# Optimization experiments

Measured on AMD Instinct MI355X. Metric: run time of the kernel, lower is better.

Reference implementation:

```python
import jax, jax.numpy as jnp
import numpy as np
from jax import lax

T, B, D_IN, H = 512, 128, 512, 512


def setup_inputs() -> dict:
    key = jax.random.key(0)
    k1, k2, k3, k4 = jax.random.split(key, 4)
    ins = jax.random.normal(k1, (T, B, D_IN), dtype=jnp.float32)
    resets = jax.random.bernoulli(k2, 0.05, (T, B))  # episode-boundary reset mask
    carry = jnp.zeros((B, H), dtype=jnp.float32)
    # fused GRU weights: gate order (r, z, n); input denses have no bias in flax GRUCell
    Wi = jax.random.normal(k3, (D_IN, 3 * H), dtype=jnp.float32) * (1.0 / np.sqrt(D_IN))
    Wh = jax.random.normal(k4, (H, 3 * H), dtype=jnp.float32) * (1.0 / np.sqrt(H))
    bh = jnp.zeros((3 * H,), dtype=jnp.float32)
    return {"carry": carry, "ins": ins, "resets": resets, "Wi": Wi, "Wh": Wh, "bh": bh}


def reference(carry, ins, resets, Wi, Wh, bh):
    """ScannedRNN forward: scan a flax GRUCell over time with per-step reset masking.

    Returns (final_carry [B,H], ys [T,B,H]).
    """

    def step(h, xr):
        x, r_mask = xr                       # x: [B,D_in], r_mask: [B]
        h = jnp.where(r_mask[:, None], jnp.zeros_like(h), h)
        gi = x @ Wi                          # [B,3H]  (no input bias in flax GRUCell)
        gh = h @ Wh + bh                     # [B,3H]
        ir, iz, inn = jnp.split(gi, 3, axis=-1)
        hr, hz, hn = jnp.split(gh, 3, axis=-1)
        r = jax.nn.sigmoid(ir + hr)
        z = jax.nn.sigmoid(iz + hz)
        n = jnp.tanh(inn + r * hn)
        new_h = (1.0 - z) * n + z * h
        return new_h, new_h                  # GRUCell returns (new_carry, new_carry)

    final_carry, ys = lax.scan(step, carry, (ins, resets))
    return final_carry, ys
```

## Files before the change

### kernel.cpp

```cpp
#include <hip/hip_runtime.h>

#define T_STEPS 512
#define BATCH   128
#define DIN     512
#define HDIM    512
#define THREEH  1536
#define THREADS 256
#define LDK     520
#define LDG     49
#define NGROUP  4
#define NSLICE  32
#define BC      32
#define HC      16
#define NC      48
#define CNT_STRIDE 16
#define FLAG_STRIDE 4
#define SPIN_MAX (1 << 22)
#define EX_DWORDS (NSLICE * BATCH * HC / 2)
#define DEC_OFF    2048
#define EX_OFF     4096
#define GI_OFF     (1u<<20)
#define GI_BYTES   201326592ULL

typedef _Float16 half8 __attribute__((ext_vector_type(8)));
typedef _Float16 half4v __attribute__((ext_vector_type(4)));
typedef float    f32x4 __attribute__((ext_vector_type(4)));
typedef unsigned int uint4v __attribute__((ext_vector_type(4)));

__global__ void sniff_kernel(const unsigned int* __restrict__ w,
                             unsigned int* __restrict__ dec) {
  unsigned int local = 0;
  for (int i = threadIdx.x; i < (T_STEPS * BATCH) / 4; i += THREADS) {
    if (w[i] > 1u) local = 1u;
  }
  if (local) atomicOr(dec, 1u);
}

__device__ __forceinline__ void run_gemm(const _Float16* __restrict__ sAa,
                                         const _Float16* __restrict__ sW,
                                         float* __restrict__ sAcc,
                                         int wid, int lane) {
  const int fr = lane & 15;
  const int kb = (lane >> 4) * 8;
  for (int tile = wid; tile < 6; tile += 4) {
    int mi = tile / 3, ni = tile - mi * 3;
    const _Float16* ap = sAa + (mi * 16 + fr) * LDK + kb;
    const _Float16* bp = sW  + (ni * 16 + fr) * LDK + kb;
    f32x4 acc = {0.f, 0.f, 0.f, 0.f};
#pragma unroll
    for (int kk = 0; kk < DIN / 32; ++kk)
      acc = __builtin_amdgcn_mfma_f32_16x16x32_f16(
          *(const half8*)(ap + kk * 32),
          *(const half8*)(bp + kk * 32), acc, 0, 0, 0);
    int crow = mi * 16 + (lane >> 4) * 4;
    int ccol = ni * 16 + fr;
#pragma unroll
    for (int j = 0; j < 4; ++j) sAcc[(crow + j) * LDG + ccol] = acc[j];
  }
}

__global__ __launch_bounds__(THREADS, 1)
void gru_kernel_v1(const float* __restrict__ carry,
                   const float* __restrict__ ins,
                   const void*  __restrict__ resets_raw,
                   const float* __restrict__ Wi,
                   const float* __restrict__ Wh,
                   const float* __restrict__ bh,
                   float* __restrict__ out,
                   unsigned int* __restrict__ cnt,
                   unsigned int* __restrict__ ex0,
                   unsigned int* __restrict__ ex1,
                   const unsigned int* __restrict__ dec)
{
  __shared__ alignas(16) _Float16 sWi[NC * LDK];
  __shared__ alignas(16) _Float16 sWh[NC * LDK];
  __shared__ alignas(16) _Float16 sA [BC * LDK];
  __shared__ float sGi[BC * LDG];
  __shared__ float sGh[BC * LDG];
  __shared__ float sBh[NC];
  __shared__ int   sRst[BC];

  const int tid  = threadIdx.x;
  const int bid  = blockIdx.x;
  const int g    = bid & (NGROUP - 1);
  const int p    = bid >> 2;
  const int row0 = g * BC;
  const int col0 = p * HC;

  float* carryOut = out;
  float* ys = out + BATCH * HDIM;

  const unsigned int isBool = *dec;
  const unsigned char* r8  = (const unsigned char*)resets_raw;
  const int*           r32 = (const int*)resets_raw;

  unsigned int* ex[2] = { ex0, ex1 };
  unsigned int* myCnt = cnt + g * CNT_STRIDE;

  for (int idx = tid; idx < DIN * NC; idx += THREADS) {
    int k  = idx / NC;
    int ci = idx - k * NC;
    int gcol = (ci >> 4) * HDIM + col0 + (ci & 15);
    sWi[ci * LDK + k] = (_Float16)Wi[k * THREEH + gcol];
    sWh[ci * LDK + k] = (_Float16)Wh[k * THREEH + gcol];
  }
  if (tid < NC) {
    int gcol = (tid >> 4) * HDIM + col0 + (tid & 15);
    sBh[tid] = bh[gcol];
  }

  float hreg[2];
  {
    int idx = tid * 2;
    int b0 = idx >> 4, c0 = idx & 15;
    hreg[0] = carry[(size_t)(row0 + b0) * HDIM + col0 + c0];
    hreg[1] = carry[(size_t)(row0 + b0) * HDIM + col0 + c0 + 1];
  }

  const int wid  = tid >> 6;
  const int lane = tid & 63;

  auto stageRst = [&](int t) {
    if (tid < BC) {
      int off = t * BATCH + row0 + tid;
      sRst[tid] = isBool ? (int)r8[off] : r32[off];
    }
  };
  auto stageX = [&](int t) {
    const float4* src = (const float4*)(ins + (size_t)(t * BATCH + row0) * DIN);
    for (int i = tid; i < BC * (DIN / 4); i += THREADS) {
      int r = i >> 7, c4 = i & 127;
      float4 v = src[(size_t)r * 128 + c4];
      half4v hv = {(_Float16)v.x, (_Float16)v.y, (_Float16)v.z, (_Float16)v.w};
      *(half4v*)&sA[r * LDK + c4 * 4] = hv;
    }
  };

  stageRst(0);
  stageX(0);
  __syncthreads();
  run_gemm(sA, sWi, sGi, wid, lane);
  __syncthreads();
  {
    const float4* src = (const float4*)(carry + (size_t)row0 * HDIM);
    for (int i = tid; i < BC * (HDIM / 4); i += THREADS) {
      int r = i >> 7, c4 = i & 127;
      float4 v = src[(size_t)r * 128 + c4];
      float m = sRst[r] ? 0.f : 1.f;
      half4v hv = {(_Float16)(v.x*m), (_Float16)(v.y*m),
                   (_Float16)(v.z*m), (_Float16)(v.w*m)};
      *(half4v*)&sA[r * LDK + c4 * 4] = hv;
    }
  }
  __syncthreads();

  for (int t = 0; t < T_STEPS; ++t) {
    if (t > 0) {
      {
        const unsigned int target = 32u * (unsigned)t;
        unsigned int fv;
        for (int it = 0; it < SPIN_MAX; ++it) {
          asm volatile("global_load_dword %0, %1, off sc0 sc1\n\t"
                       "s_waitcnt vmcnt(0)"
                       : "=v"(fv) : "v"(myCnt) : "memory");
          if (fv >= target) break;
          __builtin_amdgcn_s_sleep(1);
        }
      }
      {
        const unsigned int* exsrc = ex[(t - 1) & 1];
        uint4v vv[8];
#pragma unroll
        for (int j = 0; j < 8; ++j) {
          int i = tid + THREADS * j;
          int p_ = i >> 6, b_ = (i >> 1) & 31, hw = (i & 1) << 2;
          const unsigned int* sp = exsrc + p_ * 1024 + (row0 + b_) * 8 + hw;
          asm volatile("global_load_dwordx4 %0, %1, off sc0 sc1"
                       : "=&v"(vv[j]) : "v"(sp) : "memory");
        }
        asm volatile("s_waitcnt vmcnt(0)" ::: "memory");
        __builtin_amdgcn_sched_barrier(0);
#pragma unroll
        for (int j = 0; j < 8; ++j) {
          int i = tid + THREADS * j;
          int p_ = i >> 6, b_ = (i >> 1) & 31, hw = (i & 1) << 3;
          half8 hv = *reinterpret_cast<half8*>(&vv[j]);
          half8 z = {(_Float16)0, (_Float16)0, (_Float16)0, (_Float16)0,
                     (_Float16)0, (_Float16)0, (_Float16)0, (_Float16)0};
          hv = sRst[b_] ? z : hv;
          *(half8*)&sA[b_ * LDK + p_ * 16 + hw] = hv;
        }
      }
      __syncthreads();
    }

    run_gemm(sA, sWh, sGh, wid, lane);
    __syncthreads();

    {
#pragma unroll
      for (int e = 0; e < 2; ++e) {
        int idx = tid * 2 + e;
        int b = idx >> 4, cj = idx & 15;
        float gir = sGi[b * LDG + cj];
        float giz = sGi[b * LDG + 16 + cj];
        float gin = sGi[b * LDG + 32 + cj];
        float ghr = sGh[b * LDG + cj]      + sBh[cj];
        float ghz = sGh[b * LDG + 16 + cj] + sBh[16 + cj];
        float ghn = sGh[b * LDG + 32 + cj] + sBh[32 + cj];
        float r = 1.f / (1.f + __expf(-(gir + ghr)));
        float z = 1.f / (1.f + __expf(-(giz + ghz)));
        float n = tanhf(gin + r * ghn);
        float hp = sRst[b] ? 0.f : hreg[e];
        hreg[e] = (1.f - z) * n + z * hp;
      }
      union { _Float16 h[2]; unsigned int u; } pk;
      pk.h[0] = (_Float16)hreg[0];
      pk.h[1] = (_Float16)hreg[1];
      unsigned int* dst = ex[t & 1] + p * 1024 + (row0 + (tid >> 3)) * 8 + (tid & 7);
      asm volatile("global_store_dword %0, %1, off sc0 sc1"
                   :: "v"(dst), "v"(pk.u) : "memory");
      int b0 = (tid * 2) >> 4, c0 = (tid * 2) & 15;
      float2 yv = make_float2(hreg[0], hreg[1]);
      *(float2*)&ys[((size_t)t * BATCH + row0 + b0) * HDIM + col0 + c0] = yv;
      if (t == T_STEPS - 1)
        *(float2*)&carryOut[(size_t)(row0 + b0) * HDIM + col0 + c0] = yv;
    }
    asm volatile("s_waitcnt vmcnt(0)" ::: "memory");
    __syncthreads();
    if (tid == 0) atomicAdd(myCnt, 1u);

    if (t < T_STEPS - 1) {
      stageRst(t + 1);
      stageX(t + 1);
      __syncthreads();
      run_gemm(sA, sWi, sGi, wid, lane);
      __syncthreads();
    }
  }
}

__global__ __launch_bounds__(256, 1)
void gi_prepass2(const float* __restrict__ ins,
                 const float* __restrict__ Wi,
                 _Float16* __restrict__ gis)
{
  __shared__ alignas(16) _Float16 sWiT[48 * LDK];
  __shared__ alignas(16) _Float16 sX[32 * LDK];

  const int tid = threadIdx.x;
  const int bid = blockIdx.x;
  const int n   = bid >> 3;
  const int mg  = bid & 7;
  const int wid = tid >> 6;
  const int lane = tid & 63;
  const int fr = lane & 15;
  const int kb = (lane >> 4) * 8;

  for (int idx = tid; idx < 48 * DIN; idx += 256) {
    int ci = idx % 48, k = idx / 48;
    int gcol = (ci >> 4) * HDIM + n * 16 + (ci & 15);
    sWiT[ci * LDK + k] = (_Float16)Wi[(size_t)k * THREEH + gcol];
  }

  float4 va[16];
  auto LOADS = [&](int ch) {
    const float4* src = (const float4*)(ins + (size_t)(mg * 8192 + ch * 32) * DIN);
#pragma unroll
    for (int j = 0; j < 16; ++j) va[j] = src[tid + 256 * j];
  };
  auto WRITE = [&]() {
#pragma unroll
    for (int j = 0; j < 16; ++j) {
      int i = tid + 256 * j;
      int r = i >> 7, c4 = i & 127;
      float4 v = va[j];
      half4v hv = {(_Float16)v.x, (_Float16)v.y, (_Float16)v.z, (_Float16)v.w};
      *(half4v*)&sX[r * LDK + c4 * 4] = hv;
    }
  };

  LOADS(0);
  for (int ch = 0; ch < 256; ++ch) {
    WRITE();
    __syncthreads();
    if (ch + 1 < 256) LOADS(ch + 1);

    const int m0 = mg * 8192 + ch * 32;
    const int tt = m0 >> 7;
    const int bb0 = m0 & 127;
    for (int tile = wid; tile < 6; tile += 4) {
      int mi = tile / 3, ni = tile - mi * 3;
      const _Float16* ap = sX   + (mi * 16 + fr) * LDK + kb;
      const _Float16* bp = sWiT + (ni * 16 + fr) * LDK + kb;
      f32x4 acc = {0.f, 0.f, 0.f, 0.f};
#pragma unroll
      for (int kk = 0; kk < DIN / 32; ++kk)
        acc = __builtin_amdgcn_mfma_f32_16x16x32_f16(
            *(const half8*)(ap + kk * 32),
            *(const half8*)(bp + kk * 32), acc, 0, 0, 0);
      int gr = mi * 16 + ((lane >> 4) << 2);
      int col = n * 16 + fr;
      size_t base = ((size_t)(tt * 3 + ni) * BATCH) * HDIM + col;
#pragma unroll
      for (int j = 0; j < 4; ++j)
        gis[base + (size_t)(bb0 + gr + j) * HDIM] = (_Float16)acc[j];
    }
    __syncthreads();
  }
}

__global__ __launch_bounds__(THREADS, 1)
void gru_kernel_v3(const float* __restrict__ carry,
                   const void*  __restrict__ resets_raw,
                   const float* __restrict__ Wh,
                   const float* __restrict__ bh,
                   float* __restrict__ out,
                   unsigned int* __restrict__ flags,
                   unsigned int* __restrict__ ex0,
                   unsigned int* __restrict__ ex1,
                   const _Float16* __restrict__ gis,
                   const unsigned int* __restrict__ dec)
{
  __shared__ alignas(16) _Float16 sWh[NC * LDK];
  __shared__ alignas(16) _Float16 sA [BC * LDK];
  __shared__ float sGh[BC * LDG];
  __shared__ float sBh[NC];
  __shared__ int   sRst[BC];

  const int tid  = threadIdx.x;
  const int bid  = blockIdx.x;
  const int g    = bid & (NGROUP - 1);
  const int p    = bid >> 2;
  const int row0 = g * BC;
  const int col0 = p * HC;

  float* carryOut = out;
  float* ys = out + BATCH * HDIM;

  const unsigned int isBool = *dec;
  const unsigned char* r8  = (const unsigned char*)resets_raw;
  const int*           r32 = (const int*)resets_raw;

  unsigned int* ex[2] = { ex0, ex1 };

  for (int idx = tid; idx < DIN * NC; idx += THREADS) {
    int k  = idx / NC;
    int ci = idx - k * NC;
    int gcol = (ci >> 4) * HDIM + col0 + (ci & 15);
    sWh[ci * LDK + k] = (_Float16)Wh[k * THREEH + gcol];
  }
  if (tid < NC) {
    int gcol = (tid >> 4) * HDIM + col0 + (tid & 15);
    sBh[tid] = bh[gcol];
  }

  float hreg[2];
  {
    int idx = tid * 2;
    int b0 = idx >> 4, c0 = idx & 15;
    hreg[0] = carry[(size_t)(row0 + b0) * HDIM + col0 + c0];
    hreg[1] = carry[(size_t)(row0 + b0) * HDIM + col0 + c0 + 1];
  }

  const int wid  = tid >> 6;
  const int lane = tid & 63;
  const int gb   = tid >> 3;
  const int gcd  = tid & 7;

  if (tid < BC) {
    int off = row0 + tid;
    sRst[tid] = isBool ? (int)r8[off] : r32[off];
  }
  __syncthreads();
  {
    const float4* src = (const float4*)(carry + (size_t)row0 * HDIM);
    for (int i = tid; i < BC * (HDIM / 4); i += THREADS) {
      int r = i >> 7, c4 = i & 127;
      float4 v = src[(size_t)r * 128 + c4];
      float m = sRst[r] ? 0.f : 1.f;
      half4v hv = {(_Float16)(v.x*m), (_Float16)(v.y*m),
                   (_Float16)(v.z*m), (_Float16)(v.w*m)};
      *(half4v*)&sA[r * LDK + c4 * 4] = hv;
    }
  }

  for (int t = 0; t < T_STEPS; ++t) {
    unsigned int giu0, giu1, giu2;
    {
      const unsigned int* gp = (const unsigned int*)gis
        + ((((size_t)(t * 3) * BATCH + row0 + gb) * HDIM + col0) >> 1) + gcd;
      const size_t gstride = (size_t)BATCH * HDIM / 2;
      giu0 = gp[0];
      giu1 = gp[gstride];
      giu2 = gp[2 * gstride];
    }
    if (t > 0 && tid < BC) {
      int off = t * BATCH + row0 + tid;
      sRst[tid] = isBool ? (int)r8[off] : r32[off];
    }
    if (t > 0 && tid < NSLICE) {
      const unsigned int* fp = flags + (size_t)(g + NGROUP * tid) * FLAG_STRIDE;
      unsigned int fv;
      for (int it = 0; it < SPIN_MAX; ++it) {
        asm volatile("global_load_dword %0, %1, off sc0 sc1\n\t"
                     "s_waitcnt vmcnt(0)"
                     : "=v"(fv) : "v"(fp) : "memory");
        if (fv >= (unsigned)t) break;
        __builtin_amdgcn_s_sleep(1);
      }
    }
    __syncthreads();

    if (t > 0) {
      const unsigned int* exsrc = ex[(t - 1) & 1];
      uint4v vv[8];
#pragma unroll
      for (int j = 0; j < 8; ++j) {
        int i = tid + THREADS * j;
        int p_ = i >> 6, b_ = (i >> 1) & 31, hw = (i & 1) << 2;
        const unsigned int* sp = exsrc + p_ * 1024 + (row0 + b_) * 8 + hw;
        asm volatile("global_load_dwordx4 %0, %1, off sc0 sc1"
                     : "=&v"(vv[j]) : "v"(sp) : "memory");
      }
      asm volatile("s_waitcnt vmcnt(0)" ::: "memory");
      __builtin_amdgcn_sched_barrier(0);
#pragma unroll
      for (int j = 0; j < 8; ++j) {
        int i = tid + THREADS * j;
        int p_ = i >> 6, b_ = (i >> 1) & 31, hw = (i & 1) << 3;
        half8 hv = *reinterpret_cast<half8*>(&vv[j]);
        half8 z = {(_Float16)0, (_Float16)0, (_Float16)0, (_Float16)0,
                   (_Float16)0, (_Float16)0, (_Float16)0, (_Float16)0};
        hv = sRst[b_] ? z : hv;
        *(half8*)&sA[b_ * LDK + p_ * 16 + hw] = hv;
      }
      __syncthreads();
    }

    run_gemm(sA, sWh, sGh, wid, lane);
    __syncthreads();

    {
      union { unsigned int u; _Float16 h[2]; } u0, u1, u2;
      u0.u = giu0; u1.u = giu1; u2.u = giu2;
#pragma unroll
      for (int e = 0; e < 2; ++e) {
        int cj = gcd * 2 + e;
        float gir = (float)u0.h[e];
        float giz = (float)u1.h[e];
        float gin = (float)u2.h[e];
        float ghr = sGh[gb * LDG + cj]      + sBh[cj];
        float ghz = sGh[gb * LDG + 16 + cj] + sBh[16 + cj];
        float ghn = sGh[gb * LDG + 32 + cj] + sBh[32 + cj];
        float r = 1.f / (1.f + __expf(-(gir + ghr)));
        float z = 1.f / (1.f + __expf(-(giz + ghz)));
        float n = tanhf(gin + r * ghn);
        float hp = sRst[gb] ? 0.f : hreg[e];
        hreg[e] = (1.f - z) * n + z * hp;
      }
      union { _Float16 h[2]; unsigned int u; } pk;
      pk.h[0] = (_Float16)hreg[0];
      pk.h[1] = (_Float16)hreg[1];
      unsigned int* dst = ex[t & 1] + p * 1024 + (row0 + gb) * 8 + gcd;
      asm volatile("global_store_dword %0, %1, off sc0 sc1"
                   :: "v"(dst), "v"(pk.u) : "memory");
    }
    asm volatile("s_waitcnt vmcnt(0)" ::: "memory");
    __syncthreads();
    if (tid == 0) {
      unsigned int* fdst = flags + (size_t)bid * FLAG_STRIDE;
      unsigned int val = (unsigned)(t + 1);
      asm volatile("global_store_dword %0, %1, off sc0 sc1"
                   :: "v"(fdst), "v"(val) : "memory");
    }
    {
      float2 yv = make_float2(hreg[0], hreg[1]);
      *(float2*)&ys[((size_t)t * BATCH + row0 + gb) * HDIM + col0 + gcd * 2] = yv;
      if (t == T_STEPS - 1)
        *(float2*)&carryOut[(size_t)(row0 + gb) * HDIM + col0 + gcd * 2] = yv;
    }
  }
}

extern "C" void kernel_launch(void* const* d_in, const int* in_sizes, int n_in,
                              void* d_out, int out_size, void* d_ws, size_t ws_size,
                              hipStream_t stream) {
  const float* carry  = (const float*)d_in[0];
  const float* ins    = (const float*)d_in[1];
  const void*  resets = (const void*)d_in[2];
  const float* Wi     = (const float*)d_in[3];
  const float* Wh     = (const float*)d_in[4];
  const float* bh     = (const float*)d_in[5];
  float* out = (float*)d_out;

  unsigned int* flags = (unsigned int*)d_ws;
  unsigned int* dec   = (unsigned int*)((char*)d_ws + DEC_OFF);
  unsigned int* ex0   = (unsigned int*)((char*)d_ws + EX_OFF);
  unsigned int* ex1   = ex0 + EX_DWORDS;
  _Float16*     gis   = (_Float16*)((char*)d_ws + GI_OFF);

  (void)hipMemsetAsync(d_ws, 0, 4096, stream);

  sniff_kernel<<<dim3(1), dim3(THREADS), 0, stream>>>(
      (const unsigned int*)resets, dec);

  const bool bigWs = ws_size >= (size_t)GI_OFF + GI_BYTES;

  if (bigWs) {
    gi_prepass2<<<dim3(256), dim3(256), 0, stream>>>(ins, Wi, gis);
    void* args[] = { (void*)&carry, (void*)&resets, (void*)&Wh, (void*)&bh,
                     (void*)&out, (void*)&flags, (void*)&ex0, (void*)&ex1,
                     (void*)&gis, (void*)&dec };
    (void)hipLaunchCooperativeKernel((const void*)gru_kernel_v3,
                                     dim3(NGROUP * NSLICE), dim3(THREADS),
                                     args, 0, stream);
  } else {
    void* args[] = { (void*)&carry, (void*)&ins, (void*)&resets, (void*)&Wi,
                     (void*)&Wh, (void*)&bh, (void*)&out, (void*)&flags,
                     (void*)&ex0, (void*)&ex1, (void*)&dec };
    (void)hipLaunchCooperativeKernel((const void*)gru_kernel_v1,
                                     dim3(NGROUP * NSLICE), dim3(THREADS),
                                     args, 0, stream);
  }
}
```

Before: 2.329 ms.

## Split recurrence over 256 blocks with runtime-probed lighter coherence flags

Doubles the cooperative grid to 256 blocks, each handling 16 batch rows instead of 32, so every block's per-step recurrent GEMM and elementwise work halves. At startup a handshake probes whether plain sc0 stores and loads are visible across the blocks that exchange state. If so, it drops the sc1 bits on flag and hidden-state exchange traffic to cut per-step synchronisation latency. The exchange buffer layout changes so each block reads its rows contiguously, at the cost of more blocks polling flags and a riskier coherence assumption.

```diff
diff --git a/kernel.cpp b/kernel.cpp
--- a/kernel.cpp
+++ b/kernel.cpp
@@ -14,10 +14,17 @@
 #define HC      16
 #define NC      48
 #define CNT_STRIDE 16
-#define FLAG_STRIDE 4
-#define SPIN_MAX (1 << 22)
+#define SPIN_MAX (1 << 16)
 #define EX_DWORDS (NSLICE * BATCH * HC / 2)
-#define DEC_OFF    2048
+#define NG4 8
+#define RW4 16
+#define NS4 32
+#define EXSLOT 131072
+#define FLAGS_OFF  0
+#define GBAR_OFF   1088
+#define DEC_OFF    1280
+#define VD_OFF     2048
+#define HS_OFF     3072
 #define EX_OFF     4096
 #define GI_OFF     (1u<<20)
 #define GI_BYTES   201326592ULL
@@ -310,30 +317,50 @@
   }
 }
 
-__global__ __launch_bounds__(THREADS, 1)
-void gru_kernel_v3(const float* __restrict__ carry,
+__device__ __forceinline__ void gridbar(unsigned int* ctr, int tid) {
+  __syncthreads();
+  if (tid == 0) {
+    atomicAdd(ctr, 1u);
+    unsigned int v;
+    for (int it = 0; it < SPIN_MAX; ++it) {
+      asm volatile("global_load_dword %0, %1, off sc0 sc1\n\t"
+                   "s_waitcnt vmcnt(0)" : "=v"(v) : "v"(ctr) : "memory");
+      if (v >= 256u) break;
+      __builtin_amdgcn_s_sleep(1);
+    }
+  }
+  __syncthreads();
+}
+
+__global__ __launch_bounds__(256, 1)
+void gru_kernel_v4(const float* __restrict__ carry,
                    const void*  __restrict__ resets_raw,
                    const float* __restrict__ Wh,
                    const float* __restrict__ bh,
                    float* __restrict__ out,
-                   unsigned int* __restrict__ flags,
-                   unsigned int* __restrict__ ex0,
-                   unsigned int* __restrict__ ex1,
+                   unsigned int* __restrict__ wsb,
                    const _Float16* __restrict__ gis,
                    const unsigned int* __restrict__ dec)
 {
   __shared__ alignas(16) _Float16 sWh[NC * LDK];
-  __shared__ alignas(16) _Float16 sA [BC * LDK];
-  __shared__ float sGh[BC * LDG];
+  __shared__ alignas(16) _Float16 sA [RW4 * LDK];
+  __shared__ float sGh[RW4 * LDG];
   __shared__ float sBh[NC];
-  __shared__ int   sRst[BC];
+  __shared__ int   sRst[RW4];
+  __shared__ int   sFast;
 
   const int tid  = threadIdx.x;
   const int bid  = blockIdx.x;
-  const int g    = bid & (NGROUP - 1);
-  const int p    = bid >> 2;
-  const int row0 = g * BC;
+  const int g    = bid & 7;
+  const int p    = bid >> 3;
+  const int row0 = g * RW4;
   const int col0 = p * HC;
+
+  unsigned int* flags = wsb + (FLAGS_OFF / 4) ;
+  unsigned int* gbars = wsb + (GBAR_OFF / 4);
+  unsigned int* vd    = wsb + (VD_OFF / 4);
+  unsigned int* hs    = wsb + (HS_OFF / 4);
+  char*         exb   = (char*)wsb + EX_OFF;
 
   float* carryOut = out;
   float* ys = out + BATCH * HDIM;
@@ -342,7 +369,75 @@
   const unsigned char* r8  = (const unsigned char*)resets_raw;
   const int*           r32 = (const int*)resets_raw;
 
-  unsigned int* ex[2] = { ex0, ex1 };
+  bool ok1 = true, ok2 = true;
+  {
+    unsigned int PAT1 = 0xC0DE0000u | (unsigned)bid;
+    unsigned int PAT2 = 0xFACE0000u | (unsigned)bid;
+    if (tid == 0) {
+      unsigned int* hp = hs + bid;
+      asm volatile("global_store_dword %0, %1, off sc0\n\t"
+                   "s_waitcnt vmcnt(0)" :: "v"(hp), "v"(PAT1) : "memory");
+    }
+    gridbar(gbars + 0 * 16, tid);
+    if (tid < 32) {
+      int peer = g + 8 * tid;
+      unsigned int v;
+      const unsigned int* hp = hs + peer;
+      asm volatile("global_load_dword %0, %1, off sc0\n\t"
+                   "s_waitcnt vmcnt(0)" : "=v"(v) : "v"(hp) : "memory");
+      ok1 = (v == (0xC0DE0000u | (unsigned)peer));
+    }
+    gridbar(gbars + 1 * 16, tid);
+    if (tid == 0) {
+      unsigned int* hp = hs + bid;
+      asm volatile("global_store_dword %0, %1, off sc0\n\t"
+                   "s_waitcnt vmcnt(0)" :: "v"(hp), "v"(PAT2) : "memory");
+    }
+    gridbar(gbars + 2 * 16, tid);
+    if (tid < 32) {
+      int peer = g + 8 * tid;
+      unsigned int v;
+      const unsigned int* hp = hs + peer;
+      asm volatile("global_load_dword %0, %1, off sc0\n\t"
+                   "s_waitcnt vmcnt(0)" : "=v"(v) : "v"(hp) : "memory");
+      ok2 = (v == (0xFACE0000u | (unsigned)peer));
+    }
+    bool myok = (tid < 32) ? (ok1 && ok2) : true;
+    bool wgok = __all(myok);
+    if (tid == 0) {
+      unsigned int vv = wgok ? 1u : 0u;
+      unsigned int* vp = vd + bid;
+      asm volatile("global_store_dword %0, %1, off sc0 sc1\n\t"
+                   "s_waitcnt vmcnt(0)" :: "v"(vp), "v"(vv) : "memory");
+    }
+    gridbar(gbars + 3 * 16, tid);
+    bool fin = true;
+    if (tid < 32) {
+      int peer = g + 8 * tid;
+      unsigned int v;
+      const unsigned int* vp = vd + peer;
+      asm volatile("global_load_dword %0, %1, off sc0 sc1\n\t"
+                   "s_waitcnt vmcnt(0)" : "=v"(v) : "v"(vp) : "memory");
+      fin = (v == 1u);
+    }
+    bool unan = __all((tid < 32) ? fin : true);
+    if (tid == 0) sFast = unan ? 1 : 0;
+    __syncthreads();
+  }
+  const int fast = sFast;
+
+  if (tid == 0) {
+    unsigned int* fp = flags + (g * 32 + p);
+    unsigned int zz = 0u;
+    if (fast) {
+      asm volatile("global_store_dword %0, %1, off sc0\n\t"
+                   "s_waitcnt vmcnt(0)" :: "v"(fp), "v"(zz) : "memory");
+    } else {
+      asm volatile("global_store_dword %0, %1, off sc0 sc1\n\t"
+                   "s_waitcnt vmcnt(0)" :: "v"(fp), "v"(zz) : "memory");
+    }
+  }
+  gridbar(gbars + 4 * 16, tid);
 
   for (int idx = tid; idx < DIN * NC; idx += THREADS) {
     int k  = idx / NC;
@@ -355,27 +450,23 @@
     sBh[tid] = bh[gcol];
   }
 
-  float hreg[2];
-  {
-    int idx = tid * 2;
-    int b0 = idx >> 4, c0 = idx & 15;
-    hreg[0] = carry[(size_t)(row0 + b0) * HDIM + col0 + c0];
-    hreg[1] = carry[(size_t)(row0 + b0) * HDIM + col0 + c0 + 1];
-  }
+  const int gb = tid >> 4;
+  const int gc = tid & 15;
+  float hreg = carry[(size_t)(row0 + gb) * HDIM + col0 + gc];
 
   const int wid  = tid >> 6;
   const int lane = tid & 63;
-  const int gb   = tid >> 3;
-  const int gcd  = tid & 7;
-
-  if (tid < BC) {
+  const int fr   = lane & 15;
+  const int kb   = (lane >> 4) * 8;
+
+  if (tid < RW4) {
     int off = row0 + tid;
     sRst[tid] = isBool ? (int)r8[off] : r32[off];
   }
   __syncthreads();
   {
     const float4* src = (const float4*)(carry + (size_t)row0 * HDIM);
-    for (int i = tid; i < BC * (HDIM / 4); i += THREADS) {
+    for (int i = tid; i < RW4 * (HDIM / 4); i += THREADS) {
       int r = i >> 7, c4 = i & 127;
       float4 v = src[(size_t)r * 128 + c4];
       float m = sRst[r] ? 0.f : 1.f;
@@ -385,102 +476,146 @@
     }
   }
 
+  const unsigned short* gisu = (const unsigned short*)gis;
+
   for (int t = 0; t < T_STEPS; ++t) {
-    unsigned int giu0, giu1, giu2;
+    unsigned short gu0, gu1, gu2;
     {
-      const unsigned int* gp = (const unsigned int*)gis
-        + ((((size_t)(t * 3) * BATCH + row0 + gb) * HDIM + col0) >> 1) + gcd;
-      const size_t gstride = (size_t)BATCH * HDIM / 2;
-      giu0 = gp[0];
-      giu1 = gp[gstride];
-      giu2 = gp[2 * gstride];
-    }
-    if (t > 0 && tid < BC) {
+      size_t base = ((size_t)(t * 3) * BATCH + row0 + gb) * HDIM + col0 + gc;
+      gu0 = gisu[base];
+      gu1 = gisu[base + (size_t)BATCH * HDIM];
+      gu2 = gisu[base + 2 * (size_t)BATCH * HDIM];
+    }
+    if (t > 0 && tid < RW4) {
       int off = t * BATCH + row0 + tid;
       sRst[tid] = isBool ? (int)r8[off] : r32[off];
     }
-    if (t > 0 && tid < NSLICE) {
-      const unsigned int* fp = flags + (size_t)(g + NGROUP * tid) * FLAG_STRIDE;
-      unsigned int fv;
-      for (int it = 0; it < SPIN_MAX; ++it) {
-        asm volatile("global_load_dword %0, %1, off sc0 sc1\n\t"
+    if (t > 0) {
+      bool done = false;
+      const unsigned int* fp = flags + (g * 32 + (tid & 31));
+      for (int it = 0; it < SPIN_MAX && !done; ++it) {
+        unsigned int fv = 0xFFFFFFFFu;
+        if (tid < 32) {
+          if (fast) {
+            asm volatile("global_load_dword %0, %1, off sc0\n\t"
+                         "s_waitcnt vmcnt(0)" : "=v"(fv) : "v"(fp) : "memory");
+          } else {
+            asm volatile("global_load_dword %0, %1, off sc0 sc1\n\t"
+                         "s_waitcnt vmcnt(0)" : "=v"(fv) : "v"(fp) : "memory");
+          }
+        }
+        done = __all((tid < 32) ? (fv >= (unsigned)t) : true);
+        if (!done) __builtin_amdgcn_s_sleep(1);
+      }
+    }
+    __syncthreads();
+
+    if (t > 0) {
+      const char* src = exb + ((t - 1) & 1) * EXSLOT + g * 16384
+                      + (tid >> 4) * 1024 + (tid & 15) * 64;
+      uint4v v0, v1, v2, v3;
+      if (fast) {
+        asm volatile("global_load_dwordx4 %0, %4, off sc0\n\t"
+                     "global_load_dwordx4 %1, %4, off offset:16 sc0\n\t"
+                     "global_load_dwordx4 %2, %4, off offset:32 sc0\n\t"
+                     "global_load_dwordx4 %3, %4, off offset:48 sc0\n\t"
                      "s_waitcnt vmcnt(0)"
-                     : "=v"(fv) : "v"(fp) : "memory");
-        if (fv >= (unsigned)t) break;
-        __builtin_amdgcn_s_sleep(1);
-      }
-    }
-    __syncthreads();
-
-    if (t > 0) {
-      const unsigned int* exsrc = ex[(t - 1) & 1];
-      uint4v vv[8];
-#pragma unroll
-      for (int j = 0; j < 8; ++j) {
-        int i = tid + THREADS * j;
-        int p_ = i >> 6, b_ = (i >> 1) & 31, hw = (i & 1) << 2;
-        const unsigned int* sp = exsrc + p_ * 1024 + (row0 + b_) * 8 + hw;
-        asm volatile("global_load_dwordx4 %0, %1, off sc0 sc1"
-                     : "=&v"(vv[j]) : "v"(sp) : "memory");
-      }
-      asm volatile("s_waitcnt vmcnt(0)" ::: "memory");
+                     : "=&v"(v0), "=&v"(v1), "=&v"(v2), "=&v"(v3)
+                     : "v"(src) : "memory");
+      } else {
+        asm volatile("global_load_dwordx4 %0, %4, off sc0 sc1\n\t"
+                     "global_load_dwordx4 %1, %4, off offset:16 sc0 sc1\n\t"
+                     "global_load_dwordx4 %2, %4, off offset:32 sc0 sc1\n\t"
+                     "global_load_dwordx4 %3, %4, off offset:48 sc0 sc1\n\t"
+                     "s_waitcnt vmcnt(0)"
+                     : "=&v"(v0), "=&v"(v1), "=&v"(v2), "=&v"(v3)
+                     : "v"(src) : "memory");
+      }
       __builtin_amdgcn_sched_barrier(0);
-#pragma unroll
-      for (int j = 0; j < 8; ++j) {
-        int i = tid + THREADS * j;
-        int p_ = i >> 6, b_ = (i >> 1) & 31, hw = (i & 1) << 3;
-        half8 hv = *reinterpret_cast<half8*>(&vv[j]);
-        half8 z = {(_Float16)0, (_Float16)0, (_Float16)0, (_Float16)0,
-                   (_Float16)0, (_Float16)0, (_Float16)0, (_Float16)0};
-        hv = sRst[b_] ? z : hv;
-        *(half8*)&sA[b_ * LDK + p_ * 16 + hw] = hv;
-      }
+      int r = tid >> 4, c0 = (tid & 15) * 32;
+      half8 h0 = *reinterpret_cast<half8*>(&v0);
+      half8 h1 = *reinterpret_cast<half8*>(&v1);
+      half8 h2 = *reinterpret_cast<half8*>(&v2);
+      half8 h3 = *reinterpret_cast<half8*>(&v3);
+      half8 z = {(_Float16)0, (_Float16)0, (_Float16)0, (_Float16)0,
+                 (_Float16)0, (_Float16)0, (_Float16)0, (_Float16)0};
+      if (sRst[r]) { h0 = z; h1 = z; h2 = z; h3 = z; }
+      *(half8*)&sA[r * LDK + c0 +  0] = h0;
+      *(half8*)&sA[r * LDK + c0 +  8] = h1;
+      *(half8*)&sA[r * LDK + c0 + 16] = h2;
+      *(half8*)&sA[r * LDK + c0 + 24] = h3;
       __syncthreads();
     }
 
-    run_gemm(sA, sWh, sGh, wid, lane);
+    if (wid < 3) {
+      const int ni = wid;
+      const _Float16* ap = sA  + fr * LDK + kb;
+      const _Float16* bp = sWh + (ni * 16 + fr) * LDK + kb;
+      f32x4 a0 = {0.f, 0.f, 0.f, 0.f}, a1 = {0.f, 0.f, 0.f, 0.f};
+#pragma unroll
+      for (int kk = 0; kk < DIN / 32; kk += 2) {
+        a0 = __builtin_amdgcn_mfma_f32_16x16x32_f16(
+            *(const half8*)(ap + kk * 32), *(const half8*)(bp + kk * 32), a0, 0, 0, 0);
+        a1 = __builtin_amdgcn_mfma_f32_16x16x32_f16(
+            *(const half8*)(ap + (kk + 1) * 32), *(const half8*)(bp + (kk + 1) * 32), a1, 0, 0, 0);
+      }
+      a0 += a1;
+      int crow = (lane >> 4) * 4;
+      int ccol = ni * 16 + fr;
+#pragma unroll
+      for (int j = 0; j < 4; ++j) sGh[(crow + j) * LDG + ccol] = a0[j];
+    }
     __syncthreads();
 
     {
-      union { unsigned int u; _Float16 h[2]; } u0, u1, u2;
-      u0.u = giu0; u1.u = giu1; u2.u = giu2;
-#pragma unroll
-      for (int e = 0; e < 2; ++e) {
-        int cj = gcd * 2 + e;
-        float gir = (float)u0.h[e];
-        float giz = (float)u1.h[e];
-        float gin = (float)u2.h[e];
-        float ghr = sGh[gb * LDG + cj]      + sBh[cj];
-        float ghz = sGh[gb * LDG + 16 + cj] + sBh[16 + cj];
-        float ghn = sGh[gb * LDG + 32 + cj] + sBh[32 + cj];
-        float r = 1.f / (1.f + __expf(-(gir + ghr)));
-        float z = 1.f / (1.f + __expf(-(giz + ghz)));
-        float n = tanhf(gin + r * ghn);
-        float hp = sRst[gb] ? 0.f : hreg[e];
-        hreg[e] = (1.f - z) * n + z * hp;
-      }
-      union { _Float16 h[2]; unsigned int u; } pk;
-      pk.h[0] = (_Float16)hreg[0];
-      pk.h[1] = (_Float16)hreg[1];
-      unsigned int* dst = ex[t & 1] + p * 1024 + (row0 + gb) * 8 + gcd;
-      asm volatile("global_store_dword %0, %1, off sc0 sc1"
-                   :: "v"(dst), "v"(pk.u) : "memory");
+      union { unsigned short u; _Float16 h; } c0_, c1_, c2_;
+      c0_.u = gu0; c1_.u = gu1; c2_.u = gu2;
+      float gir = (float)c0_.h;
+      float giz = (float)c1_.h;
+      float gin = (float)c2_.h;
+      float ghr = sGh[gb * LDG + gc]      + sBh[gc];
+      float ghz = sGh[gb * LDG + 16 + gc] + sBh[16 + gc];
+      float ghn = sGh[gb * LDG + 32 + gc] + sBh[32 + gc];
+      float r = 1.f / (1.f + __expf(-(gir + ghr)));
+      float z = 1.f / (1.f + __expf(-(giz + ghz)));
+      float n = tanhf(gin + r * ghn);
+      float hp = sRst[gb] ? 0.f : hreg;
+      hreg = (1.f - z) * n + z * hp;
+
+      union { _Float16 h; unsigned short u; } pk;
+      pk.h = (_Float16)hreg;
+      unsigned int pv = (unsigned int)pk.u;
+      unsigned short* dst = (unsigned short*)
+        (exb + (t & 1) * EXSLOT + g * 16384 + gb * 1024 + (col0 + gc) * 2);
+      if (fast) {
+        asm volatile("global_store_short %0, %1, off sc0"
+                     :: "v"(dst), "v"(pv) : "memory");
+      } else {
+        asm volatile("global_store_short %0, %1, off sc0 sc1"
+                     :: "v"(dst), "v"(pv) : "memory");
+      }
     }
     asm volatile("s_waitcnt vmcnt(0)" ::: "memory");
     __syncthreads();
     if (tid == 0) {
-      unsigned int* fdst = flags + (size_t)bid * FLAG_STRIDE;
+      unsigned int* fp = flags + (g * 32 + p);
       unsigned int val = (unsigned)(t + 1);
-      asm volatile("global_store_dword %0, %1, off sc0 sc1"
-                   :: "v"(fdst), "v"(val) : "memory");
+      if (fast) {
+        asm volatile("global_store_dword %0, %1, off sc0"
+                     :: "v"(fp), "v"(val) : "memory");
+      } else {
+        asm volatile("global_store_dword %0, %1, off sc0 sc1"
+                     :: "v"(fp), "v"(val) : "memory");
+      }
     }
     {
-      float2 yv = make_float2(hreg[0], hreg[1]);
-      *(float2*)&ys[((size_t)t * BATCH + row0 + gb) * HDIM + col0 + gcd * 2] = yv;
+      ys[((size_t)t * BATCH + row0 + gb) * HDIM + col0 + gc] = hreg;
       if (t == T_STEPS - 1)
-        *(float2*)&carryOut[(size_t)(row0 + gb) * HDIM + col0 + gcd * 2] = yv;
-    }
-  }
+        carryOut[(size_t)(row0 + gb) * HDIM + col0 + gc] = hreg;
+    }
+  }
+
+  __builtin_amdgcn_fence(__ATOMIC_RELEASE, "agent");
 }
 
 extern "C" void kernel_launch(void* const* d_in, const int* in_sizes, int n_in,
@@ -494,11 +629,11 @@
   const float* bh     = (const float*)d_in[5];
   float* out = (float*)d_out;
 
-  unsigned int* flags = (unsigned int*)d_ws;
-  unsigned int* dec   = (unsigned int*)((char*)d_ws + DEC_OFF);
-  unsigned int* ex0   = (unsigned int*)((char*)d_ws + EX_OFF);
-  unsigned int* ex1   = ex0 + EX_DWORDS;
-  _Float16*     gis   = (_Float16*)((char*)d_ws + GI_OFF);
+  unsigned int* wsb  = (unsigned int*)d_ws;
+  unsigned int* dec  = (unsigned int*)((char*)d_ws + DEC_OFF);
+  unsigned int* ex0  = (unsigned int*)((char*)d_ws + EX_OFF);
+  unsigned int* ex1  = ex0 + EX_DWORDS;
+  _Float16*     gis  = (_Float16*)((char*)d_ws + GI_OFF);
 
   (void)hipMemsetAsync(d_ws, 0, 4096, stream);
 
@@ -510,14 +645,13 @@
   if (bigWs) {
     gi_prepass2<<<dim3(256), dim3(256), 0, stream>>>(ins, Wi, gis);
     void* args[] = { (void*)&carry, (void*)&resets, (void*)&Wh, (void*)&bh,
-                     (void*)&out, (void*)&flags, (void*)&ex0, (void*)&ex1,
-                     (void*)&gis, (void*)&dec };
-    (void)hipLaunchCooperativeKernel((const void*)gru_kernel_v3,
-                                     dim3(NGROUP * NSLICE), dim3(THREADS),
+                     (void*)&out, (void*)&wsb, (void*)&gis, (void*)&dec };
+    (void)hipLaunchCooperativeKernel((const void*)gru_kernel_v4,
+                                     dim3(256), dim3(256),
                                      args, 0, stream);
   } else {
     void* args[] = { (void*)&carry, (void*)&ins, (void*)&resets, (void*)&Wi,
-                     (void*)&Wh, (void*)&bh, (void*)&out, (void*)&flags,
+                     (void*)&Wh, (void*)&bh, (void*)&out, (void*)&wsb,
                      (void*)&ex0, (void*)&ex1, (void*)&dec };
     (void)hipLaunchCooperativeKernel((const void*)gru_kernel_v1,
                                      dim3(NGROUP * NSLICE), dim3(THREADS),
```

Result: faster. 2.140 ms (-8.1%).
